# Optimization experiments

Measured on AMD Instinct MI355X. Metric: run time of the kernel, lower is better.

The kernel has to match this reference:

```python
import jax, jax.numpy as jnp
import numpy as np

N_NODES = 100000
N_EDGES = 800000
D_EDGE = 64
D_NODE = 128
D_OUT = 128


def setup_inputs() -> dict:
    key = jax.random.key(0)
    ks = jax.random.split(key, 7)
    vdata = jax.random.normal(ks[0], (N_NODES, D_NODE), dtype=jnp.float32)
    edata_a = jax.random.normal(ks[1], (N_EDGES, D_EDGE), dtype=jnp.float32)
    edata_b = jax.random.normal(ks[2], (N_EDGES, D_EDGE), dtype=jnp.float32)
    conn_a = jax.random.randint(ks[3], (2, N_EDGES), 0, N_NODES, dtype=jnp.int64)
    conn_b = jax.random.randint(ks[4], (2, N_EDGES), 0, N_NODES, dtype=jnp.int64)
    d_in = 2 * D_EDGE + D_NODE  # aggregated (per-type) concat + vdata
    W = jax.random.normal(ks[5], (d_in, D_OUT), dtype=jnp.float32) / np.sqrt(d_in)
    b = jnp.zeros((D_OUT,), dtype=jnp.float32)
    return {"vdata": vdata, "edata_a": edata_a, "edata_b": edata_b,
            "conn_a": conn_a, "conn_b": conn_b, "W": W, "b": b}


def _aggregate(edata, receivers, num_nodes):
    # scatter-sum edge features into node-sized buffer (Aggregator with sum reduce)
    return jax.ops.segment_sum(edata, receivers, num_segments=num_nodes)


def reference(vdata, edata_a, edata_b, conn_a, conn_b, W, b):
    n = vdata.shape[0]
    agg_a = _aggregate(edata_a, conn_a[1, :], n)  # [N, D_EDGE]
    agg_b = _aggregate(edata_b, conn_b[1, :], n)  # [N, D_EDGE]
    x = jnp.concatenate([agg_a, agg_b, vdata], axis=1)  # [N, 2*D_EDGE + D_NODE]
    return x @ W + b  # dense updater (Linear)
```

## Files before the change

### kernel.cpp

```cpp
#include <hip/hip_runtime.h>


#define EDGES_PER_WAVE 8
#define NB 32

__global__ __launch_bounds__(256) void scatter_kernel(
    const float* __restrict__ edata, const int* __restrict__ recv,
    float* __restrict__ agg, int n_edges) {
  const int lane = threadIdx.x & 63;
  const int wave = blockIdx.x * (blockDim.x >> 6) + (threadIdx.x >> 6);
  const int e0 = wave * EDGES_PER_WAVE;

  if (e0 + EDGES_PER_WAVE <= n_edges) {
    int r[EDGES_PER_WAVE];
    float v[EDGES_PER_WAVE];
#pragma unroll
    for (int i = 0; i < EDGES_PER_WAVE; ++i) {
      const int e = e0 + i;
      r[i] = recv[e];
      v[i] = edata[(size_t)e * 64 + lane];
    }
#pragma unroll
    for (int i = 0; i < EDGES_PER_WAVE; ++i) {
      atomicAdd(&agg[(size_t)r[i] * 64 + lane], v[i]);
    }
  } else {
    for (int e = e0; e < n_edges; ++e) {
      const int r = recv[e];
      const float v = edata[(size_t)e * 64 + lane];
      atomicAdd(&agg[(size_t)r * 64 + lane], v);
    }
  }
}

__device__ __forceinline__ void fma4(float4& acc, float s, const float4& w) {
  acc.x = fmaf(s, w.x, acc.x);
  acc.y = fmaf(s, w.y, acc.y);
  acc.z = fmaf(s, w.z, acc.z);
  acc.w = fmaf(s, w.w, acc.w);
}

__global__ __launch_bounds__(256) void fused_gemm_kernel(
    const float* __restrict__ agg_a, const float* __restrict__ agg_b,
    const float* __restrict__ vdata, const float* __restrict__ W,
    const float* __restrict__ bias, float* __restrict__ out, int n_nodes) {
  __shared__ float xs[NB][260];

  const int tid = threadIdx.x;
  const int n0 = blockIdx.x * NB;

  const float4* A4 = (const float4*)(agg_a + (size_t)n0 * 64);
  const float4* B4 = (const float4*)(agg_b + (size_t)n0 * 64);
  const float4* V4 = (const float4*)(vdata + (size_t)n0 * 128);
#pragma unroll
  for (int i = tid; i < NB * 16; i += 256) {
    const int node = i >> 4;
    const int kk = (i & 15) << 2;
    *(float4*)&xs[node][kk] = A4[i];
    *(float4*)&xs[node][64 + kk] = B4[i];
  }
#pragma unroll
  for (int i = tid; i < NB * 32; i += 256) {
    const int node = i >> 5;
    const int kk = (i & 31) << 2;
    *(float4*)&xs[node][128 + kk] = V4[i];
  }
  __syncthreads();

  const int c = tid & 31;
  const int nset = tid >> 5;
  const float4* W4 = (const float4*)W;

  float4 acc0 = {0.f, 0.f, 0.f, 0.f};
  float4 acc1 = acc0, acc2 = acc0, acc3 = acc0;

#pragma unroll 4
  for (int k = 0; k < 256; k += 4) {
    const float4 w0 = W4[(k + 0) * 32 + c];
    const float4 w1 = W4[(k + 1) * 32 + c];
    const float4 w2 = W4[(k + 2) * 32 + c];
    const float4 w3 = W4[(k + 3) * 32 + c];
    const float4 x0 = *(const float4*)&xs[nset * 4 + 0][k];
    const float4 x1 = *(const float4*)&xs[nset * 4 + 1][k];
    const float4 x2 = *(const float4*)&xs[nset * 4 + 2][k];
    const float4 x3 = *(const float4*)&xs[nset * 4 + 3][k];

    fma4(acc0, x0.x, w0); fma4(acc0, x0.y, w1); fma4(acc0, x0.z, w2); fma4(acc0, x0.w, w3);
    fma4(acc1, x1.x, w0); fma4(acc1, x1.y, w1); fma4(acc1, x1.z, w2); fma4(acc1, x1.w, w3);
    fma4(acc2, x2.x, w0); fma4(acc2, x2.y, w1); fma4(acc2, x2.z, w2); fma4(acc2, x2.w, w3);
    fma4(acc3, x3.x, w0); fma4(acc3, x3.y, w1); fma4(acc3, x3.z, w2); fma4(acc3, x3.w, w3);
  }

  const float4 bb = ((const float4*)bias)[c];
  acc0.x += bb.x; acc0.y += bb.y; acc0.z += bb.z; acc0.w += bb.w;
  acc1.x += bb.x; acc1.y += bb.y; acc1.z += bb.z; acc1.w += bb.w;
  acc2.x += bb.x; acc2.y += bb.y; acc2.z += bb.z; acc2.w += bb.w;
  acc3.x += bb.x; acc3.y += bb.y; acc3.z += bb.z; acc3.w += bb.w;

  float4* O4 = (float4*)out;
  const int nb = n0 + nset * 4;
  if (nb + 3 < n_nodes) {
    O4[(size_t)(nb + 0) * 32 + c] = acc0;
    O4[(size_t)(nb + 1) * 32 + c] = acc1;
    O4[(size_t)(nb + 2) * 32 + c] = acc2;
    O4[(size_t)(nb + 3) * 32 + c] = acc3;
  } else {
    if (nb + 0 < n_nodes) O4[(size_t)(nb + 0) * 32 + c] = acc0;
    if (nb + 1 < n_nodes) O4[(size_t)(nb + 1) * 32 + c] = acc1;
    if (nb + 2 < n_nodes) O4[(size_t)(nb + 2) * 32 + c] = acc2;
    if (nb + 3 < n_nodes) O4[(size_t)(nb + 3) * 32 + c] = acc3;
  }
}

extern "C" void kernel_launch(void* const* d_in, const int* in_sizes, int n_in,
                              void* d_out, int out_size, void* d_ws, size_t ws_size,
                              hipStream_t stream) {
  const float* vdata   = (const float*)d_in[0];
  const float* edata_a = (const float*)d_in[1];
  const float* edata_b = (const float*)d_in[2];
  const int*   conn_a  = (const int*)d_in[3];
  const int*   conn_b  = (const int*)d_in[4];
  const float* W       = (const float*)d_in[5];
  const float* bias    = (const float*)d_in[6];
  float*       out     = (float*)d_out;

  const int n_nodes = in_sizes[0] / 128;
  const int n_edges = in_sizes[1] / 64;

  float* agg_a = (float*)d_ws;
  float* agg_b = agg_a + (size_t)n_nodes * 64;

  hipMemsetAsync(d_ws, 0, (size_t)n_nodes * 64 * 2 * sizeof(float), stream);

  const int waves = (n_edges + EDGES_PER_WAVE - 1) / EDGES_PER_WAVE;
  const int sblocks = (waves + 3) / 4;
  scatter_kernel<<<sblocks, 256, 0, stream>>>(edata_a, conn_a + n_edges, agg_a, n_edges);
  scatter_kernel<<<sblocks, 256, 0, stream>>>(edata_b, conn_b + n_edges, agg_b, n_edges);

  const int gblocks = (n_nodes + NB - 1) / NB;
  fused_gemm_kernel<<<gblocks, 256, 0, stream>>>(agg_a, agg_b, vdata, W, bias, out, n_nodes);
}
```

Measured before the change: 778.7 us.

## Replace float atomic scatter with counting-sort CSR and gather fused into GEMM

Instead of scattering edge features with float atomicAdd into node buffers, the code builds a per-receiver CSR index (histogram, two-level scan, permutation of edge ids) and then gathers and sums edge rows per node inside the GEMM kernel. This removes the 2x51M float atomics and the memset and round trip of the aggregate buffers. In exchange it adds several small kernels with integer atomics, and the gather reads edge rows in random order. The summation order is no longer fixed by atomics, and the per-node loop over up to max(ca,cb) edges can diverge.

```diff
diff --git a/kernel.cpp b/kernel.cpp
--- a/kernel.cpp
+++ b/kernel.cpp
@@ -1,35 +1,80 @@
 #include <hip/hip_runtime.h>
 
 
-#define EDGES_PER_WAVE 8
 #define NB 32
-
-__global__ __launch_bounds__(256) void scatter_kernel(
-    const float* __restrict__ edata, const int* __restrict__ recv,
-    float* __restrict__ agg, int n_edges) {
-  const int lane = threadIdx.x & 63;
-  const int wave = blockIdx.x * (blockDim.x >> 6) + (threadIdx.x >> 6);
-  const int e0 = wave * EDGES_PER_WAVE;
-
-  if (e0 + EDGES_PER_WAVE <= n_edges) {
-    int r[EDGES_PER_WAVE];
-    float v[EDGES_PER_WAVE];
-#pragma unroll
-    for (int i = 0; i < EDGES_PER_WAVE; ++i) {
-      const int e = e0 + i;
-      r[i] = recv[e];
-      v[i] = edata[(size_t)e * 64 + lane];
-    }
-#pragma unroll
-    for (int i = 0; i < EDGES_PER_WAVE; ++i) {
-      atomicAdd(&agg[(size_t)r[i] * 64 + lane], v[i]);
-    }
-  } else {
-    for (int e = e0; e < n_edges; ++e) {
-      const int r = recv[e];
-      const float v = edata[(size_t)e * 64 + lane];
-      atomicAdd(&agg[(size_t)r * 64 + lane], v);
-    }
+#define CHUNK 512
+#define NCHUNK_MAX 256
+
+__global__ __launch_bounds__(256) void hist_kernel(
+    const int* __restrict__ ra, const int* __restrict__ rb,
+    int* __restrict__ counts_a, int* __restrict__ counts_b, int n_edges) {
+  const int e = blockIdx.x * 256 + threadIdx.x;
+  if (e < n_edges) {
+    atomicAdd(&counts_a[ra[e]], 1);
+    atomicAdd(&counts_b[rb[e]], 1);
+  }
+}
+
+__global__ __launch_bounds__(CHUNK) void scan_chunks(
+    const int* __restrict__ counts, int* __restrict__ incl,
+    int* __restrict__ partials, int apad) {
+  __shared__ int sh[2][CHUNK];
+  const int base = blockIdx.y * apad;
+  const int i = blockIdx.x * CHUNK + threadIdx.x;
+  const int t = threadIdx.x;
+  sh[0][t] = counts[base + i];
+  __syncthreads();
+  int src = 0;
+  for (int off = 1; off < CHUNK; off <<= 1) {
+    int v = sh[src][t];
+    if (t >= off) v += sh[src][t - off];
+    sh[src ^ 1][t] = v;
+    src ^= 1;
+    __syncthreads();
+  }
+  const int inc = sh[src][t];
+  incl[base + i] = inc;
+  if (t == CHUNK - 1) partials[blockIdx.y * NCHUNK_MAX + blockIdx.x] = inc;
+}
+
+__global__ __launch_bounds__(NCHUNK_MAX) void scan_partials(
+    int* __restrict__ partials, int n_chunks) {
+  __shared__ int sh[2][NCHUNK_MAX];
+  const int base = blockIdx.y * NCHUNK_MAX;
+  const int t = threadIdx.x;
+  const int own = (t < n_chunks) ? partials[base + t] : 0;
+  sh[0][t] = own;
+  __syncthreads();
+  int src = 0;
+  for (int off = 1; off < NCHUNK_MAX; off <<= 1) {
+    int v = sh[src][t];
+    if (t >= off) v += sh[src][t - off];
+    sh[src ^ 1][t] = v;
+    src ^= 1;
+    __syncthreads();
+  }
+  if (t < n_chunks) partials[base + t] = sh[src][t] - own;
+}
+
+__global__ __launch_bounds__(CHUNK) void finalize_offsets(
+    const int* __restrict__ counts, int* __restrict__ cursor,
+    const int* __restrict__ partials, int apad) {
+  const int base = blockIdx.y * apad;
+  const int i = blockIdx.x * CHUNK + threadIdx.x;
+  cursor[base + i] = cursor[base + i] - counts[base + i] +
+                     partials[blockIdx.y * NCHUNK_MAX + blockIdx.x];
+}
+
+__global__ __launch_bounds__(256) void permute_kernel(
+    const int* __restrict__ ra, const int* __restrict__ rb,
+    int* __restrict__ cur_a, int* __restrict__ cur_b,
+    int* __restrict__ eid_a, int* __restrict__ eid_b, int n_edges) {
+  const int e = blockIdx.x * 256 + threadIdx.x;
+  if (e < n_edges) {
+    const int pa = atomicAdd(&cur_a[ra[e]], 1);
+    eid_a[pa] = e;
+    const int pb = atomicAdd(&cur_b[rb[e]], 1);
+    eid_b[pb] = e;
   }
 }
 
@@ -40,30 +85,44 @@
   acc.w = fmaf(s, w.w, acc.w);
 }
 
-__global__ __launch_bounds__(256) void fused_gemm_kernel(
-    const float* __restrict__ agg_a, const float* __restrict__ agg_b,
+__global__ __launch_bounds__(256) void fused_gather_gemm(
+    const float* __restrict__ edata_a, const float* __restrict__ edata_b,
+    const int* __restrict__ eid_a, const int* __restrict__ eid_b,
+    const int* __restrict__ end_a, const int* __restrict__ cnt_a,
+    const int* __restrict__ end_b, const int* __restrict__ cnt_b,
     const float* __restrict__ vdata, const float* __restrict__ W,
     const float* __restrict__ bias, float* __restrict__ out, int n_nodes) {
   __shared__ float xs[NB][260];
 
   const int tid = threadIdx.x;
+  const int lane = tid & 63;
+  const int wv = tid >> 6;
   const int n0 = blockIdx.x * NB;
 
-  const float4* A4 = (const float4*)(agg_a + (size_t)n0 * 64);
-  const float4* B4 = (const float4*)(agg_b + (size_t)n0 * 64);
   const float4* V4 = (const float4*)(vdata + (size_t)n0 * 128);
-#pragma unroll
-  for (int i = tid; i < NB * 16; i += 256) {
-    const int node = i >> 4;
-    const int kk = (i & 15) << 2;
-    *(float4*)&xs[node][kk] = A4[i];
-    *(float4*)&xs[node][64 + kk] = B4[i];
-  }
 #pragma unroll
   for (int i = tid; i < NB * 32; i += 256) {
     const int node = i >> 5;
     const int kk = (i & 31) << 2;
     *(float4*)&xs[node][128 + kk] = V4[i];
+  }
+
+  for (int j = 0; j < 8; ++j) {
+    const int ln = wv * 8 + j;
+    const int n = n0 + ln;
+    float sa = 0.f, sb = 0.f;
+    if (n < n_nodes) {
+      const int ea = end_a[n], ca = cnt_a[n];
+      const int eb = end_b[n], cb = cnt_b[n];
+      const int ia = ea - ca, ib = eb - cb;
+      const int m = ca > cb ? ca : cb;
+      for (int t = 0; t < m; ++t) {
+        if (t < ca) sa += edata_a[(size_t)eid_a[ia + t] * 64 + lane];
+        if (t < cb) sb += edata_b[(size_t)eid_b[ib + t] * 64 + lane];
+      }
+    }
+    xs[ln][lane] = sa;
+    xs[ln][64 + lane] = sb;
   }
   __syncthreads();
 
@@ -127,16 +186,34 @@
   const int n_nodes = in_sizes[0] / 128;
   const int n_edges = in_sizes[1] / 64;
 
-  float* agg_a = (float*)d_ws;
-  float* agg_b = agg_a + (size_t)n_nodes * 64;
-
-  hipMemsetAsync(d_ws, 0, (size_t)n_nodes * 64 * 2 * sizeof(float), stream);
-
-  const int waves = (n_edges + EDGES_PER_WAVE - 1) / EDGES_PER_WAVE;
-  const int sblocks = (waves + 3) / 4;
-  scatter_kernel<<<sblocks, 256, 0, stream>>>(edata_a, conn_a + n_edges, agg_a, n_edges);
-  scatter_kernel<<<sblocks, 256, 0, stream>>>(edata_b, conn_b + n_edges, agg_b, n_edges);
+  const int* recv_a = conn_a + n_edges;
+  const int* recv_b = conn_b + n_edges;
+
+  const int nchunks = (n_nodes + CHUNK - 1) / CHUNK;
+  const int apad = nchunks * CHUNK;
+
+  int* counts   = (int*)d_ws;
+  int* cursor   = counts + 2 * (size_t)apad;
+  int* partials = cursor + 2 * (size_t)apad;
+  int* eid      = partials + 2 * NCHUNK_MAX;
+  int* counts_a = counts;
+  int* counts_b = counts + apad;
+  int* cur_a    = cursor;
+  int* cur_b    = cursor + apad;
+  int* eid_a    = eid;
+  int* eid_b    = eid + n_edges;
+
+  hipMemsetAsync(counts, 0, (size_t)2 * apad * sizeof(int), stream);
+
+  const int eblocks = (n_edges + 255) / 256;
+  hist_kernel<<<eblocks, 256, 0, stream>>>(recv_a, recv_b, counts_a, counts_b, n_edges);
+  scan_chunks<<<dim3(nchunks, 2), CHUNK, 0, stream>>>(counts, cursor, partials, apad);
+  scan_partials<<<dim3(1, 2), NCHUNK_MAX, 0, stream>>>(partials, nchunks);
+  finalize_offsets<<<dim3(nchunks, 2), CHUNK, 0, stream>>>(counts, cursor, partials, apad);
+  permute_kernel<<<eblocks, 256, 0, stream>>>(recv_a, recv_b, cur_a, cur_b, eid_a, eid_b, n_edges);
 
   const int gblocks = (n_nodes + NB - 1) / NB;
-  fused_gemm_kernel<<<gblocks, 256, 0, stream>>>(agg_a, agg_b, vdata, W, bias, out, n_nodes);
-}
+  fused_gather_gemm<<<gblocks, 256, 0, stream>>>(
+      edata_a, edata_b, eid_a, eid_b, cur_a, counts_a, cur_b, counts_b,
+      vdata, W, bias, out, n_nodes);
+}
```

Result: slower. 1.235 ms (+58.7%).

## Replace atomic float scatter with bucketed edge lists and gather fused into GEMM

Applied to the files above, without the earlier changes.

Drops the two float-atomic scatter kernels and the node-sized aggregate buffers. A single build kernel counts incoming edges per receiver with integer atomics and stores edge ids in fixed-capacity per-node buckets, sending excess edges to an overflow list. The GEMM kernel then gathers and sums each node's edge features into shared memory before the matmul. The aim is to cut float atomic traffic and the aggregate write and re-read, at the cost of random gathers, wave-wide masked loops bounded by the largest degree among each wave's eight nodes, and a serial scan of the overflow list in every block.

```diff
diff --git a/kernel.cpp b/kernel.cpp
--- a/kernel.cpp
+++ b/kernel.cpp
@@ -1,34 +1,35 @@
 #include <hip/hip_runtime.h>
 
 
-#define EDGES_PER_WAVE 8
 #define NB 32
-
-__global__ __launch_bounds__(256) void scatter_kernel(
-    const float* __restrict__ edata, const int* __restrict__ recv,
-    float* __restrict__ agg, int n_edges) {
-  const int lane = threadIdx.x & 63;
-  const int wave = blockIdx.x * (blockDim.x >> 6) + (threadIdx.x >> 6);
-  const int e0 = wave * EDGES_PER_WAVE;
-
-  if (e0 + EDGES_PER_WAVE <= n_edges) {
-    int r[EDGES_PER_WAVE];
-    float v[EDGES_PER_WAVE];
-#pragma unroll
-    for (int i = 0; i < EDGES_PER_WAVE; ++i) {
-      const int e = e0 + i;
-      r[i] = recv[e];
-      v[i] = edata[(size_t)e * 64 + lane];
-    }
-#pragma unroll
-    for (int i = 0; i < EDGES_PER_WAVE; ++i) {
-      atomicAdd(&agg[(size_t)r[i] * 64 + lane], v[i]);
-    }
-  } else {
-    for (int e = e0; e < n_edges; ++e) {
-      const int r = recv[e];
-      const float v = edata[(size_t)e * 64 + lane];
-      atomicAdd(&agg[(size_t)r * 64 + lane], v);
+#define CAP 48
+#define OVF_MAX 65536
+
+__global__ __launch_bounds__(256) void build_kernel(
+    const int* __restrict__ ra, const int* __restrict__ rb,
+    int* __restrict__ cnt_a, int* __restrict__ cnt_b,
+    int* __restrict__ eid_a, int* __restrict__ eid_b,
+    int* __restrict__ ovf_cnt, int2* __restrict__ ovf, int n_edges) {
+  const int e = blockIdx.x * 256 + threadIdx.x;
+  if (e >= n_edges) return;
+  {
+    const int r = ra[e];
+    const int s = atomicAdd(&cnt_a[r], 1);
+    if (s < CAP) {
+      eid_a[r * CAP + s] = e;
+    } else {
+      const int k = atomicAdd(ovf_cnt, 1);
+      if (k < OVF_MAX) ovf[k] = make_int2(r, e);
+    }
+  }
+  {
+    const int r = rb[e];
+    const int s = atomicAdd(&cnt_b[r], 1);
+    if (s < CAP) {
+      eid_b[r * CAP + s] = e;
+    } else {
+      const int k = atomicAdd(ovf_cnt, 1);
+      if (k < OVF_MAX) ovf[k] = make_int2(r | 0x40000000, e);
     }
   }
 }
@@ -40,30 +41,132 @@
   acc.w = fmaf(s, w.w, acc.w);
 }
 
-__global__ __launch_bounds__(256) void fused_gemm_kernel(
-    const float* __restrict__ agg_a, const float* __restrict__ agg_b,
+__device__ __forceinline__ void macc4(float4& acc, float m, const float4& v) {
+  acc.x = fmaf(m, v.x, acc.x);
+  acc.y = fmaf(m, v.y, acc.y);
+  acc.z = fmaf(m, v.z, acc.z);
+  acc.w = fmaf(m, v.w, acc.w);
+}
+
+__global__ __launch_bounds__(256) void fused_gather_gemm(
+    const float* __restrict__ edata_a, const float* __restrict__ edata_b,
+    const int* __restrict__ eid_a, const int* __restrict__ eid_b,
+    const int* __restrict__ cnt_a, const int* __restrict__ cnt_b,
+    const int* __restrict__ ovf_cnt, const int2* __restrict__ ovf,
     const float* __restrict__ vdata, const float* __restrict__ W,
     const float* __restrict__ bias, float* __restrict__ out, int n_nodes) {
   __shared__ float xs[NB][260];
 
   const int tid = threadIdx.x;
+  const int lane = tid & 63;
+  const int wv = tid >> 6;
   const int n0 = blockIdx.x * NB;
-
-  const float4* A4 = (const float4*)(agg_a + (size_t)n0 * 64);
-  const float4* B4 = (const float4*)(agg_b + (size_t)n0 * 64);
+  const int ln0 = wv * 8;
+
+  const int nj = n0 + ln0 + (lane & 7);
+  int ca = 0, cb = 0;
+  if (nj < n_nodes) { ca = cnt_a[nj]; cb = cnt_b[nj]; }
+  ca = ca < CAP ? ca : CAP;
+  cb = cb < CAP ? cb : CAP;
+
+  int caj[8], cbj[8];
+#pragma unroll
+  for (int j = 0; j < 8; ++j) {
+    caj[j] = __builtin_amdgcn_readlane(ca, j);
+    cbj[j] = __builtin_amdgcn_readlane(cb, j);
+  }
+
+  int eA[8], eB[8];
+#pragma unroll
+  for (int j = 0; j < 8; ++j) {
+    const int n = n0 + ln0 + j;
+    eA[j] = (lane < caj[j]) ? eid_a[(size_t)n * CAP + lane] : 0;
+    eB[j] = (lane < cbj[j]) ? eid_b[(size_t)n * CAP + lane] : 0;
+  }
+
   const float4* V4 = (const float4*)(vdata + (size_t)n0 * 128);
-#pragma unroll
-  for (int i = tid; i < NB * 16; i += 256) {
-    const int node = i >> 4;
-    const int kk = (i & 15) << 2;
-    *(float4*)&xs[node][kk] = A4[i];
-    *(float4*)&xs[node][64 + kk] = B4[i];
-  }
 #pragma unroll
   for (int i = tid; i < NB * 32; i += 256) {
     const int node = i >> 5;
     const int kk = (i & 31) << 2;
     *(float4*)&xs[node][128 + kk] = V4[i];
+  }
+
+  const int g = lane >> 4;
+  const int fo = (lane & 15) << 2;
+  float4 aa[8], ab[8];
+#pragma unroll
+  for (int j = 0; j < 8; ++j) {
+    aa[j] = make_float4(0.f, 0.f, 0.f, 0.f);
+    ab[j] = make_float4(0.f, 0.f, 0.f, 0.f);
+  }
+
+  int mdeg = 0;
+#pragma unroll
+  for (int j = 0; j < 8; ++j) {
+    const int m = caj[j] > cbj[j] ? caj[j] : cbj[j];
+    mdeg = mdeg > m ? mdeg : m;
+  }
+  const int iters = (mdeg + 3) >> 2;
+
+  for (int t = 0; t < iters; ++t) {
+    const int idx = (t << 2) + g;
+#pragma unroll
+    for (int j = 0; j < 8; ++j) {
+      const int ida = __shfl(eA[j], idx);
+      const int idb = __shfl(eB[j], idx);
+      const float4 va = *(const float4*)&edata_a[(size_t)ida * 64 + fo];
+      const float4 vb = *(const float4*)&edata_b[(size_t)idb * 64 + fo];
+      const float ma = idx < caj[j] ? 1.f : 0.f;
+      const float mb = idx < cbj[j] ? 1.f : 0.f;
+      macc4(aa[j], ma, va);
+      macc4(ab[j], mb, vb);
+    }
+  }
+
+#pragma unroll
+  for (int j = 0; j < 8; ++j) {
+    aa[j].x += __shfl_xor(aa[j].x, 16); aa[j].y += __shfl_xor(aa[j].y, 16);
+    aa[j].z += __shfl_xor(aa[j].z, 16); aa[j].w += __shfl_xor(aa[j].w, 16);
+    aa[j].x += __shfl_xor(aa[j].x, 32); aa[j].y += __shfl_xor(aa[j].y, 32);
+    aa[j].z += __shfl_xor(aa[j].z, 32); aa[j].w += __shfl_xor(aa[j].w, 32);
+    ab[j].x += __shfl_xor(ab[j].x, 16); ab[j].y += __shfl_xor(ab[j].y, 16);
+    ab[j].z += __shfl_xor(ab[j].z, 16); ab[j].w += __shfl_xor(ab[j].w, 16);
+    ab[j].x += __shfl_xor(ab[j].x, 32); ab[j].y += __shfl_xor(ab[j].y, 32);
+    ab[j].z += __shfl_xor(ab[j].z, 32); ab[j].w += __shfl_xor(ab[j].w, 32);
+  }
+
+  {
+    int novf = *ovf_cnt;
+    novf = novf < OVF_MAX ? novf : OVF_MAX;
+    if (novf > 0) {
+      for (int k = 0; k < novf; ++k) {
+        const int2 o = ovf[k];
+        const int node = o.x & 0x3FFFFFFF;
+        const int chain = (o.x >> 30) & 1;
+        const int lj = node - (n0 + ln0);
+        if (0 <= lj && lj < 8) {
+          const float4 v = chain == 0
+              ? *(const float4*)&edata_a[(size_t)o.y * 64 + fo]
+              : *(const float4*)&edata_b[(size_t)o.y * 64 + fo];
+#pragma unroll
+          for (int j = 0; j < 8; ++j) {
+            if (j == lj) {
+              if (chain == 0) { aa[j].x += v.x; aa[j].y += v.y; aa[j].z += v.z; aa[j].w += v.w; }
+              else            { ab[j].x += v.x; ab[j].y += v.y; ab[j].z += v.z; ab[j].w += v.w; }
+            }
+          }
+        }
+      }
+    }
+  }
+
+  if (lane < 16) {
+#pragma unroll
+    for (int j = 0; j < 8; ++j) {
+      *(float4*)&xs[ln0 + j][fo] = aa[j];
+      *(float4*)&xs[ln0 + j][64 + fo] = ab[j];
+    }
   }
   __syncthreads();
 
@@ -127,16 +230,24 @@
   const int n_nodes = in_sizes[0] / 128;
   const int n_edges = in_sizes[1] / 64;
 
-  float* agg_a = (float*)d_ws;
-  float* agg_b = agg_a + (size_t)n_nodes * 64;
-
-  hipMemsetAsync(d_ws, 0, (size_t)n_nodes * 64 * 2 * sizeof(float), stream);
-
-  const int waves = (n_edges + EDGES_PER_WAVE - 1) / EDGES_PER_WAVE;
-  const int sblocks = (waves + 3) / 4;
-  scatter_kernel<<<sblocks, 256, 0, stream>>>(edata_a, conn_a + n_edges, agg_a, n_edges);
-  scatter_kernel<<<sblocks, 256, 0, stream>>>(edata_b, conn_b + n_edges, agg_b, n_edges);
+  const int* recv_a = conn_a + n_edges;
+  const int* recv_b = conn_b + n_edges;
+
+  int* cnt_a   = (int*)d_ws;
+  int* cnt_b   = cnt_a + n_nodes;
+  int* ovf_cnt = cnt_b + n_nodes;
+  int2* ovf    = (int2*)(ovf_cnt + 8);
+  int* eid_a   = (int*)(ovf + OVF_MAX);
+  int* eid_b   = eid_a + (size_t)n_nodes * CAP;
+
+  hipMemsetAsync(d_ws, 0, ((size_t)2 * n_nodes + 8) * sizeof(int), stream);
+
+  const int eblocks = (n_edges + 255) / 256;
+  build_kernel<<<eblocks, 256, 0, stream>>>(recv_a, recv_b, cnt_a, cnt_b,
+                                            eid_a, eid_b, ovf_cnt, ovf, n_edges);
 
   const int gblocks = (n_nodes + NB - 1) / NB;
-  fused_gemm_kernel<<<gblocks, 256, 0, stream>>>(agg_a, agg_b, vdata, W, bias, out, n_nodes);
-}
+  fused_gather_gemm<<<gblocks, 256, 0, stream>>>(
+      edata_a, edata_b, eid_a, eid_b, cnt_a, cnt_b, ovf_cnt, ovf,
+      vdata, W, bias, out, n_nodes);
+}
```

After: 749.6 us. 1.04x faster.
